# Performance work log

Hardware: AMD Instinct MI355X
Metric: run time of the kernel (lower is better)

## Reference

```python
import jax, jax.numpy as jnp
import numpy as np

B, G, A, C = 32, 2704, 3, 6
D, H, W = 1024, 52, 52
L, HID, K = 20, 512, 128


def setup_inputs() -> dict:
    key = jax.random.key(0)
    ks = jax.random.split(key, 7)
    return {
        "boxes": jax.random.normal(ks[0], (B, G, A, C), dtype=jnp.float32),
        "feature": jax.random.normal(ks[1], (B, D, H, W), dtype=jnp.float32),
        "text": jax.random.normal(ks[2], (B, L, HID), dtype=jnp.float32),
        "W_vs": jax.random.normal(ks[3], (D, HID), dtype=jnp.float32) * 0.02,
        "b_vs": jax.random.normal(ks[4], (HID,), dtype=jnp.float32) * 0.02,
        "W_tx": jax.random.normal(ks[5], (HID, HID), dtype=jnp.float32) * 0.02,
        "b_tx": jax.random.normal(ks[6], (HID,), dtype=jnp.float32) * 0.02,
        "select_num": K,
    }


def reference(boxes, feature, text, W_vs, b_vs, W_tx, b_tx, select_num):
    # objectness score: mean over anchors, channel 4  -> [B, G]
    score = jnp.mean(boxes, axis=2)[:, :, 4]
    _, idx = jax.lax.top_k(score, select_num)          # [B, K]
    # torch path builds a boolean mask then masked_select, which keeps
    # selected cells in grid order -> sort indices ascending
    idx = jnp.sort(idx, axis=1)

    # gather selected boxes: [B, K, A, C]
    sel_boxes = jnp.take_along_axis(boxes, idx[:, :, None, None], axis=1)

    b, d, h, w = feature.shape
    feat = feature.reshape(b, d, h * w).transpose(0, 2, 1)  # [B, G, D]
    sel_feat = jnp.take_along_axis(feat, idx[:, :, None], axis=1)  # [B, K, D]

    linear_feature = sel_feat @ W_vs + b_vs   # [B, K, HID]
    linear_text = text @ W_tx + b_tx          # [B, L, HID]

    # pack head inputs into a single array for baseline comparison
    out = jnp.concatenate([linear_feature, linear_text], axis=1)  # [B, K+L, HID]
    return out, sel_boxes
```

## Files before the change

kernel.cpp:

```cpp
#include <hip/hip_runtime.h>
#include <cstddef>

namespace {
constexpr int cB = 32;
constexpr int cG = 2704;
constexpr int cA = 3;
constexpr int cC = 6;
constexpr int cD = 1024;
constexpr int cL = 20;
constexpr int cH = 512;
constexpr int cK = 128;
constexpr int ROWS_OUT = cK + cL;
constexpr int FTHREADS = 512;
constexpr int CHUNK = (cG + FTHREADS - 1) / FTHREADS;
}

using u16x8 = __attribute__((ext_vector_type(8))) unsigned short;
using f32x4 = __attribute__((ext_vector_type(4))) float;
using bf16x8 = __attribute__((ext_vector_type(8))) short;

static __device__ __forceinline__ unsigned short f2bf(float f) {
  unsigned u = __float_as_uint(f);
  unsigned rounding = 0x7fffu + ((u >> 16) & 1u);
  return (unsigned short)((u + rounding) >> 16);
}
static __device__ __forceinline__ unsigned packbf(float lo, float hi) {
  return (unsigned)f2bf(lo) | ((unsigned)f2bf(hi) << 16);
}

__global__ __launch_bounds__(FTHREADS) void front_kernel(
    const float* __restrict__ boxes, const float* __restrict__ W_vs,
    const float* __restrict__ W_tx, const float* __restrict__ text,
    int* __restrict__ idx_out, float* __restrict__ out_boxes,
    unsigned short* __restrict__ Wt_vs, unsigned short* __restrict__ Wt_tx,
    unsigned short* __restrict__ text_bf) {
  __shared__ unsigned su[cG];
  __shared__ int hist[256];
  __shared__ int wsum[8];
  __shared__ int ssel[cK];
  __shared__ int s_rem;
  __shared__ unsigned s_prefix;
  __shared__ float tile[64][65];

  const int tid = threadIdx.x;
  const int lane = tid & 63;
  const int wv = tid >> 6;

  if (blockIdx.x < cB) {
    const int b = blockIdx.x;
    for (int g = tid; g < cG; g += FTHREADS) {
      const float* p = boxes + ((size_t)(b * cG + g) * cA) * cC + 4;
      float s = (p[0] + p[cC] + p[2 * cC]) * (1.0f / 3.0f);
      unsigned bits = __float_as_uint(s);
      su[g] = (bits & 0x80000000u) ? ~bits : (bits | 0x80000000u);
    }
    __syncthreads();

    int remaining = cK;
    unsigned prefix = 0;
    for (int pass = 0; pass < 4; ++pass) {
      const int shift = 24 - 8 * pass;
      if (tid < 256) hist[tid] = 0;
      __syncthreads();
      for (int g = tid; g < cG; g += FTHREADS) {
        unsigned u = su[g];
        if ((pass == 0) || ((u >> (shift + 8)) == (prefix >> (shift + 8))))
          atomicAdd(&hist[(u >> shift) & 255], 1);
      }
      __syncthreads();
      if (tid < 256) {
        int h = hist[tid];
        int x = h;
#pragma unroll
        for (int d = 1; d < 64; d <<= 1) {
          int n = __shfl_up(x, d);
          if (lane >= d) x += n;
        }
        if (lane == 63) wsum[wv] = x;
        __syncthreads();
        int off = 0, T = 0;
#pragma unroll
        for (int w = 0; w < 4; ++w) {
          int s = wsum[w];
          T += s;
          if (w < wv) off += s;
        }
        const int pincl = x + off;
        const int pexcl = pincl - h;
        const int target = T - remaining;
        if (target >= pexcl && target < pincl) {
          s_prefix = prefix | ((unsigned)tid << shift);
          s_rem = remaining - (T - pincl);
        }
      } else {
        __syncthreads();
      }
      __syncthreads();
      remaining = s_rem;
      prefix = s_prefix;
    }

    const int g0 = tid * CHUNK;
    const int g1 = min(g0 + CHUNK, cG);
    int cgt = 0, ceq = 0;
    for (int g = g0; g < g1; ++g) {
      unsigned u = su[g];
      cgt += (u > prefix);
      ceq += (u == prefix);
    }
    int packed = (cgt << 16) | ceq;
    int x = packed;
#pragma unroll
    for (int d = 1; d < 64; d <<= 1) {
      int n = __shfl_up(x, d);
      if (lane >= d) x += n;
    }
    if (lane == 63) wsum[wv] = x;
    __syncthreads();
    int off = 0;
#pragma unroll
    for (int w = 0; w < 8; ++w)
      if (w < wv) off += wsum[w];
    const int excl = x + off - packed;
    int gt_before = excl >> 16;
    int eq_before = excl & 0xffff;

    for (int g = g0; g < g1; ++g) {
      unsigned u = su[g];
      if (u > prefix) {
        ssel[gt_before + min(eq_before, remaining)] = g;
        ++gt_before;
      } else if (u == prefix) {
        if (eq_before < remaining) ssel[gt_before + eq_before] = g;
        ++eq_before;
      }
    }
    __syncthreads();

    if (tid < cK) idx_out[b * cK + tid] = ssel[tid];
    for (int t2 = tid; t2 < cK * (cA * cC); t2 += FTHREADS) {
      const int k = t2 / 18;
      const int e = t2 - k * 18;
      out_boxes[(size_t)(b * cK + k) * 18 + e] =
          boxes[((size_t)(b * cG) + ssel[k]) * 18 + e];
    }
  } else {
    const int t = blockIdx.x - cB;
    if (t < 128) {
      const int k0 = (t >> 3) * 64, n0 = (t & 7) * 64;
      for (int i = tid; i < 1024; i += FTHREADS) {
        const int kk = i >> 4, c4 = (i & 15) * 4;
        const float4 v =
            *(const float4*)(W_vs + (size_t)(k0 + kk) * cH + n0 + c4);
        tile[kk][c4 + 0] = v.x;
        tile[kk][c4 + 1] = v.y;
        tile[kk][c4 + 2] = v.z;
        tile[kk][c4 + 3] = v.w;
      }
      __syncthreads();
      for (int j = tid; j < 2048; j += FTHREADS) {
        const int nn = j >> 5, p = j & 31;
        unsigned v = packbf(tile[2 * p][nn], tile[2 * p + 1][nn]);
        *(unsigned*)(Wt_vs + (size_t)(n0 + nn) * cD + k0 + 2 * p) = v;
      }
    } else if (t < 192) {
      const int t2 = t - 128;
      const int k0 = (t2 >> 3) * 64, n0 = (t2 & 7) * 64;
      for (int i = tid; i < 1024; i += FTHREADS) {
        const int kk = i >> 4, c4 = (i & 15) * 4;
        const float4 v =
            *(const float4*)(W_tx + (size_t)(k0 + kk) * cH + n0 + c4);
        tile[kk][c4 + 0] = v.x;
        tile[kk][c4 + 1] = v.y;
        tile[kk][c4 + 2] = v.z;
        tile[kk][c4 + 3] = v.w;
      }
      __syncthreads();
      for (int j = tid; j < 2048; j += FTHREADS) {
        const int nn = j >> 5, p = j & 31;
        unsigned v = packbf(tile[2 * p][nn], tile[2 * p + 1][nn]);
        *(unsigned*)(Wt_tx + (size_t)(n0 + nn) * cH + k0 + 2 * p) = v;
      }
    } else {
      const int t3 = t - 192;
      const size_t base = (size_t)t3 * 4096;
      for (int i = tid; i < 1024; i += FTHREADS) {
        const float4 v = *(const float4*)(text + base + (size_t)i * 4);
        uint2 pv;
        pv.x = packbf(v.x, v.y);
        pv.y = packbf(v.z, v.w);
        *(uint2*)(text_bf + base + (size_t)i * 4) = pv;
      }
    }
  }
}

template <int KD>
__device__ __forceinline__ void mfma_gemm_body(
    const unsigned short* __restrict__ A, const unsigned short* __restrict__ Bt,
    const float* __restrict__ bias, float* __restrict__ out, int bm, int bn,
    int rpb, int row_off, unsigned short (*As)[128][40],
    unsigned short (*Bs)[128][40]) {
  constexpr int NT = KD / 32;
  const int tid = threadIdx.x;
  const int wid = tid >> 6, lane = tid & 63;
  const int wr = wid >> 2, wc = wid & 3;
  const int lr = lane & 15, lg = lane >> 4;

  const int srow = tid >> 2;
  const int sc = (tid & 3) * 8;

  const unsigned short* pA = A + (size_t)(bm * 128 + srow) * KD + sc;
  const unsigned short* pB = Bt + (size_t)(bn * 128 + srow) * KD + sc;

  f32x4 acc[4][2];
#pragma unroll
  for (int i = 0; i < 4; ++i)
#pragma unroll
    for (int j = 0; j < 2; ++j) acc[i][j] = {0.f, 0.f, 0.f, 0.f};

  u16x8 xa, xb;
  u16x8 ya, yb;

#define LOAD_X(kt)                      \
  xa = *(const u16x8*)(pA + (kt) * 32); \
  xb = *(const u16x8*)(pB + (kt) * 32);
#define LOAD_Y(kt)                      \
  ya = *(const u16x8*)(pA + (kt) * 32); \
  yb = *(const u16x8*)(pB + (kt) * 32);
#define STORE_X(buf)                \
  *(u16x8*)&As[buf][srow][sc] = xa; \
  *(u16x8*)&Bs[buf][srow][sc] = xb;
#define STORE_Y(buf)                \
  *(u16x8*)&As[buf][srow][sc] = ya; \
  *(u16x8*)&Bs[buf][srow][sc] = yb;
#define COMPUTE(buf)                                                        \
  {                                                                         \
    bf16x8 af[4], bfr[2];                                                   \
    _Pragma("unroll") for (int fr = 0; fr < 4; ++fr) af[fr] =               \
        *(const bf16x8*)&As[buf][wr * 64 + fr * 16 + lr][lg * 8];           \
    _Pragma("unroll") for (int fc = 0; fc < 2; ++fc) bfr[fc] =              \
        *(const bf16x8*)&Bs[buf][wc * 32 + fc * 16 + lr][lg * 8];           \
    _Pragma("unroll") for (int fr = 0; fr < 4; ++fr)                        \
        _Pragma("unroll") for (int fc = 0; fc < 2; ++fc) acc[fr][fc] =      \
            __builtin_amdgcn_mfma_f32_16x16x32_bf16(af[fr], bfr[fc],        \
                                                    acc[fr][fc], 0, 0, 0);  \
  }

  LOAD_X(0);
  LOAD_Y(1);
  STORE_X(0);
  __syncthreads();

  for (int t = 0; t < NT; t += 2) {
    if (t + 2 < NT) LOAD_X(t + 2);
    COMPUTE(0);
    STORE_Y(1);
    __syncthreads();
    if (t + 3 < NT) LOAD_Y(t + 3);
    COMPUTE(1);
    if (t + 2 < NT) STORE_X(0);
    __syncthreads();
  }
#undef LOAD_X
#undef LOAD_Y
#undef STORE_X
#undef STORE_Y
#undef COMPUTE

  float biasv[2];
#pragma unroll
  for (int fc = 0; fc < 2; ++fc)
    biasv[fc] = bias[bn * 128 + wc * 32 + fc * 16 + lr];

#pragma unroll
  for (int fr = 0; fr < 4; ++fr) {
#pragma unroll
    for (int fc = 0; fc < 2; ++fc) {
      const int col = bn * 128 + wc * 32 + fc * 16 + lr;
#pragma unroll
      for (int j = 0; j < 4; ++j) {
        const int row = bm * 128 + wr * 64 + fr * 16 + lg * 4 + j;
        const int bb = row / rpb;
        const int rr = row - bb * rpb;
        out[(size_t)bb * (ROWS_OUT * cH) + (size_t)(row_off + rr) * cH + col] =
            acc[fr][fc][j] + biasv[fc];
      }
    }
  }
}

__global__ __launch_bounds__(512) void mid_kernel(
    const float* __restrict__ feature, const int* __restrict__ idx,
    unsigned short* __restrict__ selfeat,
    const unsigned short* __restrict__ text_bf,
    const unsigned short* __restrict__ Wt_tx, const float* __restrict__ b_tx,
    float* __restrict__ out) {
  __shared__ __align__(16) unsigned short As[2][128][40];
  __shared__ __align__(16) unsigned short Bs[2][128][40];
  const int blk = blockIdx.x;
  const int tid = threadIdx.x;

  if (blk < 1024) {
    const int kc = blk & 1;
    const int dc = (blk >> 1) & 15;
    const int b = blk >> 5;
    const int lane = tid & 63;
    const int grp = tid >> 6;
    int* sidx = (int*)&Bs[0][0][0];
    float(*tile)[65] = (float(*)[65]) & As[0][0][0];

    if (tid < 64) sidx[tid] = idx[b * cK + kc * 64 + tid];
    __syncthreads();

    const int g = sidx[lane];
    const float* fptr =
        feature + (size_t)b * cD * cG + (size_t)(dc * 64 + grp * 8) * cG + g;
    float f[8];
#pragma unroll
    for (int j = 0; j < 8; ++j) f[j] = fptr[(size_t)j * cG];
#pragma unroll
    for (int j = 0; j < 8; ++j) tile[grp * 8 + j][lane] = f[j];
    __syncthreads();

    const size_t obase = ((size_t)(b * cK + kc * 64)) * cD + dc * 64;
#pragma unroll
    for (int it = 0; it < 2; ++it) {
      const int i = tid + it * 512;
      const int kk = i >> 4;
      const int q = i & 15;
      uint2 pv;
      pv.x = packbf(tile[4 * q + 0][kk], tile[4 * q + 1][kk]);
      pv.y = packbf(tile[4 * q + 2][kk], tile[4 * q + 3][kk]);
      *(uint2*)(selfeat + obase + (size_t)kk * cD + 4 * q) = pv;
    }
  } else {
    const int t = blk - 1024;
    mfma_gemm_body<512>(text_bf, Wt_tx, b_tx, out, t >> 2, t & 3, cL, cK, As,
                        Bs);
  }
}

__global__ __launch_bounds__(512) void gemm1_kernel(
    const unsigned short* __restrict__ selfeat,
    const unsigned short* __restrict__ Wt_vs, const float* __restrict__ b_vs,
    float* __restrict__ out) {
  __shared__ __align__(16) unsigned short As[2][128][40];
  __shared__ __align__(16) unsigned short Bs[2][128][40];
  const int w = ((blockIdx.x & 7) << 4) | (blockIdx.x >> 3);
  mfma_gemm_body<1024>(selfeat, Wt_vs, b_vs, out, w >> 2, w & 3, 128, 0, As,
                       Bs);
}

extern "C" void kernel_launch(void* const* d_in, const int* in_sizes, int n_in,
                              void* d_out, int out_size, void* d_ws,
                              size_t ws_size, hipStream_t stream) {
  const float* boxes = (const float*)d_in[0];
  const float* feature = (const float*)d_in[1];
  const float* text = (const float*)d_in[2];
  const float* W_vs = (const float*)d_in[3];
  const float* b_vs = (const float*)d_in[4];
  const float* W_tx = (const float*)d_in[5];
  const float* b_tx = (const float*)d_in[6];

  float* out = (float*)d_out;
  float* out_boxes = out + (size_t)cB * ROWS_OUT * cH;

  int* idx = (int*)d_ws;
  unsigned short* selfeat = (unsigned short*)((char*)d_ws + 16384);
  unsigned short* Wt_vs = (unsigned short*)((char*)d_ws + 8404992);
  unsigned short* Wt_tx = (unsigned short*)((char*)d_ws + 9453568);
  unsigned short* text_bf = (unsigned short*)((char*)d_ws + 9977856);

  front_kernel<<<cB + 272, FTHREADS, 0, stream>>>(
      boxes, W_vs, W_tx, text, idx, out_boxes, Wt_vs, Wt_tx, text_bf);

  mid_kernel<<<1044, 512, 0, stream>>>(feature, idx, selfeat, text_bf, Wt_tx,
                                       b_tx, out);

  gemm1_kernel<<<128, 512, 0, stream>>>(selfeat, Wt_vs, b_vs, out);
}
```

Before: 82.43 us.

## Fuse gather and feature GEMM into one kernel with per-batch completion counters

Merges the feature gather/convert stage and the visual GEMM into a single persistent-style kernel of 256-thread blocks. Gather blocks loop over four work items and bump a per-batch atomic counter, and GEMM blocks spin on that counter before starting, so the GEMM for one batch can overlap gathering for later batches. The GEMM body drops its double-buffered LDS pipeline for a single-buffer loop with 4 waves each computing a 64x64 tile. This saves a kernel launch boundary and lets the stages overlap, at the cost of spin-wait blocks occupying CUs, a possible deadlock if waiting blocks get scheduled before the gather blocks they depend on, and less load/compute overlap inside the GEMM.

```diff
diff --git a/kernel.cpp b/kernel.cpp
--- a/kernel.cpp
+++ b/kernel.cpp
@@ -33,7 +33,7 @@
     const float* __restrict__ W_tx, const float* __restrict__ text,
     int* __restrict__ idx_out, float* __restrict__ out_boxes,
     unsigned short* __restrict__ Wt_vs, unsigned short* __restrict__ Wt_tx,
-    unsigned short* __restrict__ text_bf) {
+    unsigned short* __restrict__ text_bf, int* __restrict__ cnt) {
   __shared__ unsigned su[cG];
   __shared__ int hist[256];
   __shared__ int wsum[8];
@@ -146,6 +146,7 @@
     }
   } else {
     const int t = blockIdx.x - cB;
+    if (t == 0 && tid < cB) cnt[tid] = 0;
     if (t < 128) {
       const int k0 = (t >> 3) * 64, n0 = (t & 7) * 64;
       for (int i = tid; i < 1024; i += FTHREADS) {
@@ -199,85 +200,64 @@
 __device__ __forceinline__ void mfma_gemm_body(
     const unsigned short* __restrict__ A, const unsigned short* __restrict__ Bt,
     const float* __restrict__ bias, float* __restrict__ out, int bm, int bn,
-    int rpb, int row_off, unsigned short (*As)[128][40],
-    unsigned short (*Bs)[128][40]) {
+    int rpb, int row_off, unsigned short (*As)[40], unsigned short (*Bs)[40]) {
   constexpr int NT = KD / 32;
   const int tid = threadIdx.x;
   const int wid = tid >> 6, lane = tid & 63;
-  const int wr = wid >> 2, wc = wid & 3;
+  const int wr = wid >> 1, wc = wid & 1;
   const int lr = lane & 15, lg = lane >> 4;
 
   const int srow = tid >> 2;
   const int sc = (tid & 3) * 8;
 
-  const unsigned short* pA = A + (size_t)(bm * 128 + srow) * KD + sc;
-  const unsigned short* pB = Bt + (size_t)(bn * 128 + srow) * KD + sc;
-
-  f32x4 acc[4][2];
+  const unsigned short* pA0 = A + (size_t)(bm * 128 + srow) * KD + sc;
+  const unsigned short* pA1 = pA0 + (size_t)64 * KD;
+  const unsigned short* pB0 = Bt + (size_t)(bn * 128 + srow) * KD + sc;
+  const unsigned short* pB1 = pB0 + (size_t)64 * KD;
+
+  f32x4 acc[4][4];
 #pragma unroll
   for (int i = 0; i < 4; ++i)
 #pragma unroll
-    for (int j = 0; j < 2; ++j) acc[i][j] = {0.f, 0.f, 0.f, 0.f};
-
-  u16x8 xa, xb;
-  u16x8 ya, yb;
-
-#define LOAD_X(kt)                      \
-  xa = *(const u16x8*)(pA + (kt) * 32); \
-  xb = *(const u16x8*)(pB + (kt) * 32);
-#define LOAD_Y(kt)                      \
-  ya = *(const u16x8*)(pA + (kt) * 32); \
-  yb = *(const u16x8*)(pB + (kt) * 32);
-#define STORE_X(buf)                \
-  *(u16x8*)&As[buf][srow][sc] = xa; \
-  *(u16x8*)&Bs[buf][srow][sc] = xb;
-#define STORE_Y(buf)                \
-  *(u16x8*)&As[buf][srow][sc] = ya; \
-  *(u16x8*)&Bs[buf][srow][sc] = yb;
-#define COMPUTE(buf)                                                        \
-  {                                                                         \
-    bf16x8 af[4], bfr[2];                                                   \
-    _Pragma("unroll") for (int fr = 0; fr < 4; ++fr) af[fr] =               \
-        *(const bf16x8*)&As[buf][wr * 64 + fr * 16 + lr][lg * 8];           \
-    _Pragma("unroll") for (int fc = 0; fc < 2; ++fc) bfr[fc] =              \
-        *(const bf16x8*)&Bs[buf][wc * 32 + fc * 16 + lr][lg * 8];           \
-    _Pragma("unroll") for (int fr = 0; fr < 4; ++fr)                        \
-        _Pragma("unroll") for (int fc = 0; fc < 2; ++fc) acc[fr][fc] =      \
-            __builtin_amdgcn_mfma_f32_16x16x32_bf16(af[fr], bfr[fc],        \
-                                                    acc[fr][fc], 0, 0, 0);  \
+    for (int j = 0; j < 4; ++j) acc[i][j] = {0.f, 0.f, 0.f, 0.f};
+
+  for (int t = 0; t < NT; ++t) {
+    const u16x8 a0 = *(const u16x8*)(pA0 + t * 32);
+    const u16x8 a1 = *(const u16x8*)(pA1 + t * 32);
+    const u16x8 b0 = *(const u16x8*)(pB0 + t * 32);
+    const u16x8 b1 = *(const u16x8*)(pB1 + t * 32);
+    *(u16x8*)&As[srow][sc] = a0;
+    *(u16x8*)&As[srow + 64][sc] = a1;
+    *(u16x8*)&Bs[srow][sc] = b0;
+    *(u16x8*)&Bs[srow + 64][sc] = b1;
+    __syncthreads();
+
+    bf16x8 af[4], bfr[4];
+#pragma unroll
+    for (int fr = 0; fr < 4; ++fr)
+      af[fr] = *(const bf16x8*)&As[wr * 64 + fr * 16 + lr][lg * 8];
+#pragma unroll
+    for (int fc = 0; fc < 4; ++fc)
+      bfr[fc] = *(const bf16x8*)&Bs[wc * 64 + fc * 16 + lr][lg * 8];
+#pragma unroll
+    for (int fr = 0; fr < 4; ++fr)
+#pragma unroll
+      for (int fc = 0; fc < 4; ++fc)
+        acc[fr][fc] = __builtin_amdgcn_mfma_f32_16x16x32_bf16(
+            af[fr], bfr[fc], acc[fr][fc], 0, 0, 0);
+    __syncthreads();
   }
 
-  LOAD_X(0);
-  LOAD_Y(1);
-  STORE_X(0);
-  __syncthreads();
-
-  for (int t = 0; t < NT; t += 2) {
-    if (t + 2 < NT) LOAD_X(t + 2);
-    COMPUTE(0);
-    STORE_Y(1);
-    __syncthreads();
-    if (t + 3 < NT) LOAD_Y(t + 3);
-    COMPUTE(1);
-    if (t + 2 < NT) STORE_X(0);
-    __syncthreads();
-  }
-#undef LOAD_X
-#undef LOAD_Y
-#undef STORE_X
-#undef STORE_Y
-#undef COMPUTE
-
-  float biasv[2];
-#pragma unroll
-  for (int fc = 0; fc < 2; ++fc)
-    biasv[fc] = bias[bn * 128 + wc * 32 + fc * 16 + lr];
+  float biasv[4];
+#pragma unroll
+  for (int fc = 0; fc < 4; ++fc)
+    biasv[fc] = bias[bn * 128 + wc * 64 + fc * 16 + lr];
 
 #pragma unroll
   for (int fr = 0; fr < 4; ++fr) {
 #pragma unroll
-    for (int fc = 0; fc < 2; ++fc) {
-      const int col = bn * 128 + wc * 32 + fc * 16 + lr;
+    for (int fc = 0; fc < 4; ++fc) {
+      const int col = bn * 128 + wc * 64 + fc * 16 + lr;
 #pragma unroll
       for (int j = 0; j < 4; ++j) {
         const int row = bm * 128 + wr * 64 + fr * 16 + lg * 4 + j;
@@ -290,66 +270,81 @@
   }
 }
 
-__global__ __launch_bounds__(512) void mid_kernel(
+__global__ __launch_bounds__(256, 3) void fused_kernel(
     const float* __restrict__ feature, const int* __restrict__ idx,
     unsigned short* __restrict__ selfeat,
+    const unsigned short* __restrict__ Wt_vs, const float* __restrict__ b_vs,
     const unsigned short* __restrict__ text_bf,
     const unsigned short* __restrict__ Wt_tx, const float* __restrict__ b_tx,
-    float* __restrict__ out) {
-  __shared__ __align__(16) unsigned short As[2][128][40];
-  __shared__ __align__(16) unsigned short Bs[2][128][40];
+    float* __restrict__ out, int* __restrict__ cnt) {
+  __shared__ __align__(16) unsigned char smem[20480 + 256];
+  unsigned short(*As)[40] = (unsigned short(*)[40])smem;
+  unsigned short(*Bs)[40] = (unsigned short(*)[40])(smem + 10240);
+
   const int blk = blockIdx.x;
   const int tid = threadIdx.x;
 
-  if (blk < 1024) {
-    const int kc = blk & 1;
-    const int dc = (blk >> 1) & 15;
-    const int b = blk >> 5;
+  if (blk < 512) {
+    float(*tile)[65] = (float(*)[65])smem;
+    int* sidx = (int*)(smem + 20480);
     const int lane = tid & 63;
     const int grp = tid >> 6;
-    int* sidx = (int*)&Bs[0][0][0];
-    float(*tile)[65] = (float(*)[65]) & As[0][0][0];
-
-    if (tid < 64) sidx[tid] = idx[b * cK + kc * 64 + tid];
-    __syncthreads();
-
-    const int g = sidx[lane];
-    const float* fptr =
-        feature + (size_t)b * cD * cG + (size_t)(dc * 64 + grp * 8) * cG + g;
-    float f[8];
-#pragma unroll
-    for (int j = 0; j < 8; ++j) f[j] = fptr[(size_t)j * cG];
-#pragma unroll
-    for (int j = 0; j < 8; ++j) tile[grp * 8 + j][lane] = f[j];
-    __syncthreads();
-
-    const size_t obase = ((size_t)(b * cK + kc * 64)) * cD + dc * 64;
-#pragma unroll
-    for (int it = 0; it < 2; ++it) {
-      const int i = tid + it * 512;
-      const int kk = i >> 4;
-      const int q = i & 15;
-      uint2 pv;
-      pv.x = packbf(tile[4 * q + 0][kk], tile[4 * q + 1][kk]);
-      pv.y = packbf(tile[4 * q + 2][kk], tile[4 * q + 3][kk]);
-      *(uint2*)(selfeat + obase + (size_t)kk * cD + 4 * q) = pv;
-    }
-  } else {
-    const int t = blk - 1024;
+
+#pragma unroll 1
+    for (int s = 0; s < 4; ++s) {
+      const int T = s * 512 + blk;
+      const int b = T >> 6;
+      const int r = T & 63;
+      const int kc = r & 1;
+      const int dq = r >> 1;
+
+      if (tid < 64) sidx[tid] = idx[b * cK + kc * 64 + tid];
+      __syncthreads();
+
+      const int g = sidx[lane];
+      const float* fptr = feature + (size_t)b * cD * cG +
+                          (size_t)(dq * 32 + grp * 8) * cG + g;
+      float f[8];
+#pragma unroll
+      for (int j = 0; j < 8; ++j) f[j] = fptr[(size_t)j * cG];
+#pragma unroll
+      for (int j = 0; j < 8; ++j) tile[grp * 8 + j][lane] = f[j];
+      __syncthreads();
+
+      const size_t obase = ((size_t)(b * cK + kc * 64)) * cD + dq * 32;
+#pragma unroll
+      for (int it = 0; it < 2; ++it) {
+        const int i = tid + it * 256;
+        const int kk = i >> 3;
+        const int q = i & 7;
+        unsigned lo = packbf(tile[4 * q + 0][kk], tile[4 * q + 1][kk]);
+        unsigned hi = packbf(tile[4 * q + 2][kk], tile[4 * q + 3][kk]);
+        unsigned long long pv = ((unsigned long long)hi << 32) | lo;
+        __hip_atomic_store(
+            (unsigned long long*)(selfeat + obase + (size_t)kk * cD + 4 * q),
+            pv, __ATOMIC_RELAXED, __HIP_MEMORY_SCOPE_AGENT);
+      }
+      __syncthreads();
+      if (tid == 0)
+        __hip_atomic_fetch_add(&cnt[b], 1, __ATOMIC_RELEASE,
+                               __HIP_MEMORY_SCOPE_AGENT);
+    }
+  } else if (blk < 532) {
+    const int t = blk - 512;
     mfma_gemm_body<512>(text_bf, Wt_tx, b_tx, out, t >> 2, t & 3, cL, cK, As,
                         Bs);
+  } else {
+    const int r = blk - 532;
+    const int bm = r >> 2, bn = r & 3;
+    if (tid == 0) {
+      while (__hip_atomic_load(&cnt[bm], __ATOMIC_ACQUIRE,
+                               __HIP_MEMORY_SCOPE_AGENT) < 64)
+        __builtin_amdgcn_s_sleep(8);
+    }
+    __syncthreads();
+    __builtin_amdgcn_fence(__ATOMIC_ACQUIRE, "agent");
+    mfma_gemm_body<1024>(selfeat, Wt_vs, b_vs, out, bm, bn, 128, 0, As, Bs);
   }
-}
-
-__global__ __launch_bounds__(512) void gemm1_kernel(
-    const unsigned short* __restrict__ selfeat,
-    const unsigned short* __restrict__ Wt_vs, const float* __restrict__ b_vs,
-    float* __restrict__ out) {
-  __shared__ __align__(16) unsigned short As[2][128][40];
-  __shared__ __align__(16) unsigned short Bs[2][128][40];
-  const int w = ((blockIdx.x & 7) << 4) | (blockIdx.x >> 3);
-  mfma_gemm_body<1024>(selfeat, Wt_vs, b_vs, out, w >> 2, w & 3, 128, 0, As,
-                       Bs);
 }
 
 extern "C" void kernel_launch(void* const* d_in, const int* in_sizes, int n_in,
@@ -371,12 +366,11 @@
   unsigned short* Wt_vs = (unsigned short*)((char*)d_ws + 8404992);
   unsigned short* Wt_tx = (unsigned short*)((char*)d_ws + 9453568);
   unsigned short* text_bf = (unsigned short*)((char*)d_ws + 9977856);
+  int* cnt = (int*)((char*)d_ws + 10633216);
 
   front_kernel<<<cB + 272, FTHREADS, 0, stream>>>(
-      boxes, W_vs, W_tx, text, idx, out_boxes, Wt_vs, Wt_tx, text_bf);
-
-  mid_kernel<<<1044, 512, 0, stream>>>(feature, idx, selfeat, text_bf, Wt_tx,
-                                       b_tx, out);
-
-  gemm1_kernel<<<128, 512, 0, stream>>>(selfeat, Wt_vs, b_vs, out);
-}
+      boxes, W_vs, W_tx, text, idx, out_boxes, Wt_vs, Wt_tx, text_bf, cnt);
+
+  fused_kernel<<<660, 256, 0, stream>>>(feature, idx, selfeat, Wt_vs, b_vs,
+                                        text_bf, Wt_tx, b_tx, out, cnt);
+}
```

New measurement: 196.1 us. 138% more time.
